# Kernel tuning notes

Measured on AMD Instinct MI355X. Metric: run time of the kernel, lower is better.

The kernel has to match this reference:

```python
import jax, jax.numpy as jnp
import numpy as np

B, T, L = 64, 128, 32          # batch, read timesteps, item_len (write phase)
D, R = 256, 1024               # output_dim (= input dim per step), controller rnn_size
N, M = 512, 128                # memory_rows, memory_columns
RH, WH = 1, 1                  # read / write heads
EPS = 1e-8
SCALE = 0.02


def setup_inputs() -> dict:
    key = jax.random.key(0)
    ks = jax.random.split(key, 6)
    in_dim = D + RH * M                      # controller sees [x_t, prev reads]
    head_dim = RH * (M + 6) + WH * (3 * M + 6)  # k,beta,g,s(3),gamma (+erase,add for write)
    return {
        "inputs": jax.random.normal(ks[0], (B, T, D), jnp.float32),
        "W_lstm": jax.random.normal(ks[1], (in_dim, 4 * R), jnp.float32) * SCALE,
        "U_lstm": jax.random.normal(ks[2], (R, 4 * R), jnp.float32) * SCALE,
        "b_lstm": jnp.zeros((4 * R,), jnp.float32),
        "W_heads": jax.random.normal(ks[3], (R, head_dim), jnp.float32) * SCALE,
        "b_heads": jnp.zeros((head_dim,), jnp.float32),
        "W_out": jax.random.normal(ks[4], (R + RH * M, D), jnp.float32) * SCALE,
        "b_out": jnp.zeros((D,), jnp.float32),
    }


def _address(Mem, Mem_norm, k, beta, g, s, gamma, w_prev):
    """NTM content + location addressing. Mem:[B,N,M], returns w:[B,N]."""
    k = jnp.tanh(k)                                   # [B,M]
    beta = jax.nn.softplus(beta)                      # [B,1]
    g = jax.nn.sigmoid(g)                             # [B,1]
    s = jax.nn.softmax(s, axis=-1)                    # [B,3] shifts (-1,0,1)
    gamma = 1.0 + jax.nn.softplus(gamma)              # [B,1]
    # cosine similarity content addressing
    sim = jnp.einsum('bnm,bm->bn', Mem, k) / (
        Mem_norm * jnp.linalg.norm(k, axis=-1, keepdims=True) + EPS)
    w_c = jax.nn.softmax(beta * sim, axis=-1)
    # interpolate with previous weighting
    w_g = g * w_c + (1.0 - g) * w_prev
    # circular convolutional shift over {-1,0,1}
    w_s = (s[:, 0:1] * jnp.roll(w_g, -1, axis=-1)
           + s[:, 1:2] * w_g
           + s[:, 2:3] * jnp.roll(w_g, 1, axis=-1))
    # sharpen
    w_pow = (w_s + EPS) ** gamma
    return w_pow / jnp.sum(w_pow, axis=-1, keepdims=True)


def _run(inputs, W_lstm, U_lstm, b_lstm, W_heads, b_heads, W_out, b_out):
    def step(carry, x_t):
        h, c, reads, w_r, w_w, Mem = carry
        # LSTM controller
        z = jnp.concatenate([x_t, reads], -1) @ W_lstm + h @ U_lstm + b_lstm
        zi, zf, zg, zo = jnp.split(z, 4, axis=-1)
        c = jax.nn.sigmoid(zf) * c + jax.nn.sigmoid(zi) * jnp.tanh(zg)
        h = jax.nn.sigmoid(zo) * jnp.tanh(c)
        # head parameters
        p = h @ W_heads + b_heads
        Mem_norm = jnp.linalg.norm(Mem, axis=-1)  # [B,N]
        new_w_r, new_reads = [], []
        for hh in range(RH):
            o = hh * (M + 6)
            w = _address(Mem, Mem_norm, p[:, o:o + M], p[:, o + M:o + M + 1],
                         p[:, o + M + 1:o + M + 2], p[:, o + M + 2:o + M + 5],
                         p[:, o + M + 5:o + M + 6], w_r[:, hh])
            new_w_r.append(w)
            new_reads.append(jnp.einsum('bn,bnm->bm', w, Mem))
        base, wsz = RH * (M + 6), 3 * M + 6
        new_w_w = []
        for hh in range(WH):
            o = base + hh * wsz
            w = _address(Mem, Mem_norm, p[:, o:o + M], p[:, o + M:o + M + 1],
                         p[:, o + M + 1:o + M + 2], p[:, o + M + 2:o + M + 5],
                         p[:, o + M + 5:o + M + 6], w_w[:, hh])
            erase = jax.nn.sigmoid(p[:, o + M + 6:o + 2 * M + 6])
            add = jnp.tanh(p[:, o + 2 * M + 6:o + 3 * M + 6])
            Mem = Mem * (1.0 - w[:, :, None] * erase[:, None, :]) + w[:, :, None] * add[:, None, :]
            new_w_w.append(w)
        reads = jnp.concatenate(new_reads, -1)
        out = jnp.concatenate([h, reads], -1) @ W_out + b_out
        carry = (h, c, reads, jnp.stack(new_w_r, 1), jnp.stack(new_w_w, 1), Mem)
        return carry, out

    init = (jnp.zeros((B, R)), jnp.zeros((B, R)), jnp.zeros((B, RH * M)),
            jnp.full((B, RH, N), 1.0 / N), jnp.full((B, WH, N), 1.0 / N),
            jnp.full((B, N, M), 1e-6))
    # read phase (inputs) followed by write phase (zero response sheet)
    xs = jnp.concatenate([inputs, jnp.zeros((B, L, D), inputs.dtype)], axis=1)
    xs = jnp.moveaxis(xs, 0, 1)  # [T+L, B, D]
    _, outs = jax.lax.scan(step, init, xs)
    write_outputs = jax.nn.sigmoid(jnp.moveaxis(outs[T:], 0, 1))  # [B, L, D]
    return write_outputs


def reference(inputs, W_lstm, U_lstm, b_lstm, W_heads, b_heads, W_out, b_out):
    return _run(inputs, W_lstm, U_lstm, b_lstm, W_heads, b_heads, W_out, b_out)
```

## Files before the change

### kernel.cpp

```cpp
#include <hip/hip_runtime.h>
#include <hip/hip_fp16.h>
#include <math.h>

#define B 64
#define T_READ 128
#define L_WRITE 32
#define TT 160
#define D 256
#define R 1024
#define N 512
#define M 128
#define HD 524
#define K5K 1152
#define EPS 1e-8f
#define BNM ((size_t)B*N*M)

__device__ __forceinline__ float sigmoidf(float x){ return 1.0f/(1.0f+expf(-x)); }
__device__ __forceinline__ float softplusf(float x){ return (x > 20.f) ? x : log1pf(expf(x)); }

__global__ __launch_bounds__(256) void kx_transpose(const float* __restrict__ x, float* __restrict__ xT){
    __shared__ float tile[64][65];
    const int t = blockIdx.x >> 2, k0 = (blockIdx.x & 3)*64;
    #pragma unroll
    for (int rep = 0; rep < 16; ++rep){
        int idx = rep*256 + threadIdx.x;
        int bl = idx >> 6, kl = idx & 63;
        tile[bl][kl] = x[((size_t)bl*T_READ + t)*D + k0 + kl];
    }
    __syncthreads();
    #pragma unroll
    for (int rep = 0; rep < 16; ++rep){
        int idx = rep*256 + threadIdx.x;
        int kl = idx >> 6, bl = idx & 63;
        xT[((size_t)t*D + k0 + kl)*64 + bl] = tile[bl][kl];
    }
}

__global__ __launch_bounds__(256) void kpack_w(const float* __restrict__ Wl, const float* __restrict__ Ul,
                                               __half* __restrict__ Wreh){
    const int k = blockIdx.x;
    const float* src = (k < 384) ? (Wl + (size_t)k*4096) : (Ul + (size_t)(k-384)*4096);
    #pragma unroll
    for (int it = 0; it < 16; ++it){
        int j = it*256 + threadIdx.x;
        int bk = j >> 4, r = j & 15, q = r >> 2, i = r & 3;
        Wreh[((size_t)bk*1408 + k)*16 + r] = __float2half_rn(src[q*1024 + bk*4 + i]);
    }
}

__global__ __launch_bounds__(256) void kpack_wh(const float* __restrict__ Wh, __half* __restrict__ Whh){
    const int k = blockIdx.x;
    for (int j = threadIdx.x; j < HD; j += 256)
        Whh[(size_t)k*HD + j] = __float2half_rn(Wh[(size_t)k*HD + j]);
}

__global__ void k_init(float* ht, float* c_t, float* reads_fin, float* wst, __half* Mem){
    size_t idx = (size_t)blockIdx.x*blockDim.x + threadIdx.x;
    size_t stride = (size_t)gridDim.x*blockDim.x;
    const __half mi = __float2half(1e-6f);
    for (size_t i = idx; i < BNM; i += stride) Mem[i] = mi;
    for (size_t i = idx; i < R*64; i += stride){ ht[i]=0.f; c_t[i]=0.f; }
    for (size_t i = idx; i < 2*128*64; i += stride) reads_fin[i] = 0.f;
    for (size_t i = idx; i < 4*B*N; i += stride) wst[i] = 1.f/512.f;
}

__global__ __launch_bounds__(1024) void k1_z(
    const float* __restrict__ xT, const __half* __restrict__ Wreh, const float* __restrict__ bl,
    float* __restrict__ ht, float* __restrict__ c_t, const float* __restrict__ reads_fin,
    float* __restrict__ hist, int t)
{
    __shared__ float comb[16384];
    const int bk = blockIdx.x;
    const int tid = threadIdx.x, lane = tid & 63, w = tid >> 6;
    const float* rf = reads_fin + (size_t)(t & 1)*8192;

    if (t > T_READ && bk < 8){
        int e = bk*1024 + tid;
        hist[((size_t)(t-1-T_READ)*K5K + 1024 + (e>>6))*64 + (e&63)] = rf[e];
    }

    const int r0 = bk*4;
    const int rd = (t < T_READ);
    const int kn = rd ? 88 : 72;
    const int k0 = rd ? w*88 : 256 + w*72;
    const __half* wbase = Wreh + ((size_t)bk*1408 + k0)*16;
    float acc[16];
    #pragma unroll
    for (int i = 0; i < 16; ++i) acc[i] = 0.f;
    #pragma unroll 4
    for (int kk = 0; kk < kn; ++kk){
        int k = k0 + kk;
        float a;
        if (k < 256)      a = xT[((size_t)t*256 + k)*64 + lane];
        else if (k < 384) a = rf[(k-256)*64 + lane];
        else              a = ht[(size_t)(k-384)*64 + lane];
        float4 raw0 = *reinterpret_cast<const float4*>(wbase + (size_t)kk*16);
        float4 raw1 = *reinterpret_cast<const float4*>(wbase + (size_t)kk*16 + 8);
        const __half2* h0 = reinterpret_cast<const __half2*>(&raw0);
        const __half2* h1 = reinterpret_cast<const __half2*>(&raw1);
        float2 f;
        f = __half22float2(h0[0]); acc[0] += a*f.x; acc[1] += a*f.y;
        f = __half22float2(h0[1]); acc[2] += a*f.x; acc[3] += a*f.y;
        f = __half22float2(h0[2]); acc[4] += a*f.x; acc[5] += a*f.y;
        f = __half22float2(h0[3]); acc[6] += a*f.x; acc[7] += a*f.y;
        f = __half22float2(h1[0]); acc[8] += a*f.x; acc[9] += a*f.y;
        f = __half22float2(h1[1]); acc[10]+= a*f.x; acc[11]+= a*f.y;
        f = __half22float2(h1[2]); acc[12]+= a*f.x; acc[13]+= a*f.y;
        f = __half22float2(h1[3]); acc[14]+= a*f.x; acc[15]+= a*f.y;
    }
    #pragma unroll
    for (int j = 0; j < 16; ++j) comb[(w*16 + j)*64 + lane] = acc[j];
    __syncthreads();
    if (tid < 256){
        int i = tid >> 6, b2 = tid & 63;
        float g4[4];
        #pragma unroll
        for (int q = 0; q < 4; ++q){
            float s = bl[q*1024 + r0 + i];
            #pragma unroll
            for (int ks = 0; ks < 16; ++ks) s += comb[(ks*16 + q*4 + i)*64 + b2];
            g4[q] = s;
        }
        int ri = (r0 + i)*64 + b2;
        float cn = sigmoidf(g4[1])*c_t[ri] + sigmoidf(g4[0])*tanhf(g4[2]);
        float hn = sigmoidf(g4[3])*tanhf(cn);
        c_t[ri] = cn;
        ht[ri] = hn;
        if (t >= T_READ) hist[((size_t)(t-T_READ)*K5K + r0 + i)*64 + b2] = hn;
    }
}

__global__ __launch_bounds__(1024) void k2f(
    const float* __restrict__ ht, const __half* __restrict__ Whh, const float* __restrict__ bh,
    float* __restrict__ khat, float* __restrict__ scal, float* __restrict__ eal)
{
    __shared__ float part[16][2][64];
    const int tid = threadIdx.x, lane = tid & 63, w = tid >> 6;
    const int col0 = blockIdx.x*2;
    const int k0 = w*64;
    float a0 = 0.f, a1 = 0.f;
    #pragma unroll 4
    for (int k = k0; k < k0+64; ++k){
        float a = ht[(size_t)k*64 + lane];
        __half2 wv = *reinterpret_cast<const __half2*>(Whh + (size_t)k*HD + col0);
        float2 f = __half22float2(wv);
        a0 += a*f.x; a1 += a*f.y;
    }
    part[w][0][lane] = a0;
    part[w][1][lane] = a1;
    __syncthreads();
    if (tid < 128){
        int c = tid >> 6, b = tid & 63;
        int col = col0 + c;
        float v = bh[col];
        #pragma unroll
        for (int w2 = 0; w2 < 16; ++w2) v += part[w2][c][b];
        if (col < 128)       khat[b*256 + col] = tanhf(v);
        else if (col < 134){ int i = col-128; scal[b*16 + i]     = (i==0)?softplusf(v):(i==1)?sigmoidf(v):(i==5)?1.f+softplusf(v):v; }
        else if (col < 262)  khat[b*256 + 128 + (col-134)] = tanhf(v);
        else if (col < 268){ int i = col-262; scal[b*16 + 8 + i] = (i==0)?softplusf(v):(i==1)?sigmoidf(v):(i==5)?1.f+softplusf(v):v; }
        else if (col < 396)  eal[b*256 + (col-268)]        = sigmoidf(v);
        else                 eal[b*256 + 128 + (col-396)]  = tanhf(v);
    }
}

__global__ __launch_bounds__(512) void k3_dots(
    const float* __restrict__ khat, const __half* __restrict__ Mem,
    float* __restrict__ mnorm, float* __restrict__ dots, float* __restrict__ reads_fin, int t)
{
    __shared__ float kh[256];
    const int b = blockIdx.x >> 3, nq = blockIdx.x & 7;
    const int tid = threadIdx.x, lane = tid & 63, w = tid >> 6;
    if (blockIdx.x < 8){
        int e = blockIdx.x*1024 + tid;
        reads_fin[(size_t)(t & 1)*8192 + e] = 0.f;
        reads_fin[(size_t)(t & 1)*8192 + e + 512] = 0.f;
    }
    if (tid < 256) kh[tid] = khat[b*256 + tid];
    __syncthreads();
    float2 kr  = reinterpret_cast<const float2*>(kh)[lane];
    float2 kw2 = reinterpret_cast<const float2*>(kh + 128)[lane];
    #pragma unroll 2
    for (int i = 0; i < 8; ++i){
        int n = nq*64 + w*8 + i;
        const __half* mrow = Mem + ((size_t)b*N + n)*M;
        __half2 mh = *reinterpret_cast<const __half2*>(mrow + lane*2);
        float2 mv = __half22float2(mh);
        float s2 = mv.x*mv.x + mv.y*mv.y;
        float dr = mv.x*kr.x + mv.y*kr.y;
        float dw = mv.x*kw2.x + mv.y*kw2.y;
        #pragma unroll
        for (int off = 32; off; off >>= 1){
            s2 += __shfl_xor(s2, off);
            dr += __shfl_xor(dr, off);
            dw += __shfl_xor(dw, off);
        }
        if (lane == 0){
            mnorm[b*N + n] = sqrtf(s2);
            dots[(b*2+0)*N + n] = dr;
            dots[(b*2+1)*N + n] = dw;
        }
    }
}

__device__ __forceinline__ float blk_sum8g(float v, volatile float* red8, int lane, int wgi){
    #pragma unroll
    for (int off = 32; off; off >>= 1) v += __shfl_xor(v, off);
    if (lane == 0) red8[wgi] = v;
    __syncthreads();
    float r = red8[0]+red8[1]+red8[2]+red8[3]+red8[4]+red8[5]+red8[6]+red8[7];
    __syncthreads();
    return r;
}
__device__ __forceinline__ float blk_max8g(float v, volatile float* red8, int lane, int wgi){
    #pragma unroll
    for (int off = 32; off; off >>= 1) v = fmaxf(v, __shfl_xor(v, off));
    if (lane == 0) red8[wgi] = v;
    __syncthreads();
    float r = fmaxf(fmaxf(fmaxf(red8[0],red8[1]),fmaxf(red8[2],red8[3])),
                    fmaxf(fmaxf(red8[4],red8[5]),fmaxf(red8[6],red8[7])));
    __syncthreads();
    return r;
}

__global__ __launch_bounds__(1024) void k4_addr(
    const float* __restrict__ khat, const float* __restrict__ scal, const float* __restrict__ ealg,
    const float* __restrict__ mnorm, const float* __restrict__ dots,
    float* __restrict__ wst, __half* __restrict__ Mem, float* __restrict__ reads_fin, int t)
{
    __shared__ float kh[256];
    __shared__ float sc[16];
    __shared__ float eal[256];
    __shared__ float wfin[1024];
    __shared__ float wgbuf[1024];
    __shared__ float red8[2][8];
    __shared__ float racc_s[1024];
    const int b = blockIdx.x >> 3, nq = blockIdx.x & 7;
    const int tid = threadIdx.x, lane = tid & 63;

    if (tid < 256)      kh[tid]      = khat[b*256 + tid];
    else if (tid < 272) sc[tid-256]  = scal[b*16 + (tid-256)];
    else if (tid < 528) eal[tid-272] = ealg[b*256 + (tid-272)];
    __syncthreads();

    {
        const int g = tid >> 9;
        const int n = tid & 511;
        const int wgi = (tid >> 6) & 7;
        float* wgl = wgbuf + g*512;
        volatile float* r8 = red8[g];

        float kv = (n < 128) ? kh[g*128 + n] : 0.f;
        float knm = sqrtf(blk_sum8g(kv*kv, r8, lane, wgi));
        float beta = sc[g*8+0], gg = sc[g*8+1], gamma = sc[g*8+5];
        float s0r = sc[g*8+2], s1r = sc[g*8+3], s2r = sc[g*8+4];
        float smx = fmaxf(s0r, fmaxf(s1r, s2r));
        float e0 = expf(s0r-smx), e1 = expf(s1r-smx), e2 = expf(s2r-smx);
        float esum = e0+e1+e2;
        float s0 = e0/esum, s1 = e1/esum, s2 = e2/esum;

        float sim = dots[(b*2+g)*N + n] / (mnorm[b*N + n]*knm + EPS);
        float aa = beta * sim;
        float amax = blk_max8g(aa, r8, lane, wgi);
        float ev = expf(aa - amax);
        float wc = ev / blk_sum8g(ev, r8, lane, wgi);

        const float* wpr = wst + ((size_t)((t&1)*2 + g))*(B*N);
        float*       wnx = wst + ((size_t)(((t+1)&1)*2 + g))*(B*N);
        float wprev = wpr[b*N + n];
        float wgv = gg*wc + (1.f - gg)*wprev;
        wgl[n] = wgv; __syncthreads();
        float wsv = s0*wgl[(n+1)&511] + s1*wgv + s2*wgl[(n-1)&511];
        float wp2 = powf(wsv + EPS, gamma);
        float wsum = blk_sum8g(wp2, r8, lane, wgi);
        float wv = wp2 / wsum;
        wfin[g*512 + n] = wv;
        if (nq == 0) wnx[b*N + n] = wv;
        __syncthreads();
    }

    {
        const int m = tid & 127, ns = tid >> 7;
        const float e  = eal[m];
        const float ad = eal[128 + m];
        float racc = 0.f;
        #pragma unroll 4
        for (int i2 = 0; i2 < 8; ++i2){
            int nn = nq*64 + i2*8 + ns;
            size_t idx = ((size_t)b*N + nn)*M + m;
            float v = __half2float(Mem[idx]);
            float wr = wfin[nn], ww = wfin[512 + nn];
            racc += wr*v;
            Mem[idx] = __float2half_rn(v*(1.f - ww*e) + ww*ad);
        }
        racc_s[tid] = racc;
        __syncthreads();
        if (tid < 128){
            float s = 0.f;
            #pragma unroll
            for (int g2 = 0; g2 < 8; ++g2) s += racc_s[g2*128 + tid];
            atomicAdd(&reads_fin[(size_t)((t+1) & 1)*8192 + tid*64 + b], s);
        }
    }
}

__global__ __launch_bounds__(256) void k_fin(const float* __restrict__ reads_fin, float* __restrict__ hist){
    int e = blockIdx.x*256 + threadIdx.x;
    float s = reads_fin[(size_t)(TT & 1)*8192 + e];
    hist[((size_t)31*K5K + 1024 + (e>>6))*64 + (e&63)] = s;
}

__global__ __launch_bounds__(512) void k5_out(
    const float* __restrict__ hist, const float* __restrict__ Wo, const float* __restrict__ bo,
    float* __restrict__ out)
{
    __shared__ float smem[16384];
    const int tid = threadIdx.x, lane = tid & 63, w = tid >> 6;
    const int l = blockIdx.x >> 3, jg = blockIdx.x & 7;
    const int j0 = jg*32;
    float acc[32];
    #pragma unroll
    for (int i = 0; i < 32; ++i) acc[i] = 0.f;
    const int k0 = w*144;
    #pragma unroll 2
    for (int kk = 0; kk < 144; ++kk){
        int k = k0 + kk;
        float a = hist[((size_t)l*K5K + k)*64 + lane];
        const float* wrow = Wo + (size_t)k*D + j0;
        #pragma unroll
        for (int qq = 0; qq < 8; ++qq){
            float4 wv = *reinterpret_cast<const float4*>(wrow + qq*4);
            acc[qq*4+0] += a*wv.x; acc[qq*4+1] += a*wv.y;
            acc[qq*4+2] += a*wv.z; acc[qq*4+3] += a*wv.w;
        }
    }
    __syncthreads();
    #pragma unroll
    for (int c = 0; c < 32; ++c) smem[(w*32 + c)*64 + lane] = acc[c];
    __syncthreads();
    {
        const int b2 = tid >> 3, jq = tid & 7;
        float4 ov;
        float* po = (float*)&ov;
        #pragma unroll
        for (int i = 0; i < 4; ++i){
            int c = jq*4 + i;
            float s = bo[j0 + c];
            #pragma unroll
            for (int ks = 0; ks < 8; ++ks) s += smem[(ks*32 + c)*64 + b2];
            po[i] = sigmoidf(s);
        }
        *reinterpret_cast<float4*>(out + ((size_t)b2*L_WRITE + l)*D + j0 + jq*4) = ov;
    }
}

extern "C" void kernel_launch(void* const* d_in, const int* in_sizes, int n_in,
                              void* d_out, int out_size, void* d_ws, size_t ws_size,
                              hipStream_t stream)
{
    const float* x   = (const float*)d_in[0];
    const float* Wl  = (const float*)d_in[1];
    const float* Ul  = (const float*)d_in[2];
    const float* bl  = (const float*)d_in[3];
    const float* Wh  = (const float*)d_in[4];
    const float* bh  = (const float*)d_in[5];
    const float* Wo  = (const float*)d_in[6];
    const float* bo  = (const float*)d_in[7];
    float* out = (float*)d_out;

    float* ws = (float*)d_ws;
    float* xT    = ws; ws += (size_t)T_READ*D*64;
    __half* Wreh = (__half*)ws; ws += (size_t)1408*4096/2;
    __half* Whh  = (__half*)ws; ws += (size_t)1024*HD/2 + 64;
    float* ht    = ws; ws += (size_t)R*64;
    float* c_t   = ws; ws += (size_t)R*64;
    float* khat  = ws; ws += (size_t)B*256;
    float* scal  = ws; ws += (size_t)B*16;
    float* eal   = ws; ws += (size_t)B*256;
    float* mnorm = ws; ws += (size_t)B*N;
    float* dots  = ws; ws += (size_t)B*2*N;
    float* wst   = ws; ws += (size_t)4*B*N;
    __half* Mem  = (__half*)ws; ws += BNM/2;
    float* reads_fin = ws; ws += (size_t)2*128*64;
    float* hist  = ws; ws += (size_t)L_WRITE*K5K*64;

    hipLaunchKernelGGL(kx_transpose, dim3(T_READ*4), dim3(256), 0, stream, x, xT);
    hipLaunchKernelGGL(kpack_w,      dim3(1408),     dim3(256), 0, stream, Wl, Ul, Wreh);
    hipLaunchKernelGGL(kpack_wh,     dim3(1024),     dim3(256), 0, stream, Wh, Whh);
    hipLaunchKernelGGL(k_init,       dim3(2048),     dim3(256), 0, stream, ht, c_t, reads_fin, wst, Mem);

    for (int t = 0; t < TT; ++t){
        hipLaunchKernelGGL(k1_z,    dim3(256), dim3(1024), 0, stream, xT, Wreh, bl, ht, c_t, reads_fin, hist, t);
        hipLaunchKernelGGL(k2f,     dim3(262), dim3(1024), 0, stream, ht, Whh, bh, khat, scal, eal);
        hipLaunchKernelGGL(k3_dots, dim3(512), dim3(512),  0, stream, khat, Mem, mnorm, dots, reads_fin, t);
        hipLaunchKernelGGL(k4_addr, dim3(512), dim3(1024), 0, stream, khat, scal, eal, mnorm, dots, wst, Mem, reads_fin, t);
    }
    hipLaunchKernelGGL(k_fin,  dim3(32),  dim3(256), 0, stream, reads_fin, hist);
    hipLaunchKernelGGL(k5_out, dim3(256), dim3(512), 0, stream, hist, Wo, bo, out);
}
```

Baseline: 10.63 ms.

## Fuse memory-row dot products into the addressing kernel and drop k3

Removes the separate k3_dots launch. Each addressing block now computes the row norms and the key dot products for all 512 memory rows of its batch directly into shared memory. This saves one kernel launch per timestep and the global write/read round trip for mnorm and dots. The cost is that each of the 8 blocks per batch re-reads the full memory matrix for its batch, so memory traffic per step rises about 8x; those reads may be served from cache. Zeroing of reads_fin moves into k2f.

```diff
diff --git a/kernel.cpp b/kernel.cpp
--- a/kernel.cpp
+++ b/kernel.cpp
@@ -132,11 +132,16 @@
 
 __global__ __launch_bounds__(1024) void k2f(
     const float* __restrict__ ht, const __half* __restrict__ Whh, const float* __restrict__ bh,
-    float* __restrict__ khat, float* __restrict__ scal, float* __restrict__ eal)
+    float* __restrict__ khat, float* __restrict__ scal, float* __restrict__ eal,
+    float* __restrict__ reads_fin, int t)
 {
     __shared__ float part[16][2][64];
     const int tid = threadIdx.x, lane = tid & 63, w = tid >> 6;
     const int col0 = blockIdx.x*2;
+    if (blockIdx.x < 8){
+        int e = blockIdx.x*1024 + tid;
+        reads_fin[(size_t)(t & 1)*8192 + e] = 0.f;
+    }
     const int k0 = w*64;
     float a0 = 0.f, a1 = 0.f;
     #pragma unroll 4
@@ -164,45 +169,6 @@
     }
 }
 
-__global__ __launch_bounds__(512) void k3_dots(
-    const float* __restrict__ khat, const __half* __restrict__ Mem,
-    float* __restrict__ mnorm, float* __restrict__ dots, float* __restrict__ reads_fin, int t)
-{
-    __shared__ float kh[256];
-    const int b = blockIdx.x >> 3, nq = blockIdx.x & 7;
-    const int tid = threadIdx.x, lane = tid & 63, w = tid >> 6;
-    if (blockIdx.x < 8){
-        int e = blockIdx.x*1024 + tid;
-        reads_fin[(size_t)(t & 1)*8192 + e] = 0.f;
-        reads_fin[(size_t)(t & 1)*8192 + e + 512] = 0.f;
-    }
-    if (tid < 256) kh[tid] = khat[b*256 + tid];
-    __syncthreads();
-    float2 kr  = reinterpret_cast<const float2*>(kh)[lane];
-    float2 kw2 = reinterpret_cast<const float2*>(kh + 128)[lane];
-    #pragma unroll 2
-    for (int i = 0; i < 8; ++i){
-        int n = nq*64 + w*8 + i;
-        const __half* mrow = Mem + ((size_t)b*N + n)*M;
-        __half2 mh = *reinterpret_cast<const __half2*>(mrow + lane*2);
-        float2 mv = __half22float2(mh);
-        float s2 = mv.x*mv.x + mv.y*mv.y;
-        float dr = mv.x*kr.x + mv.y*kr.y;
-        float dw = mv.x*kw2.x + mv.y*kw2.y;
-        #pragma unroll
-        for (int off = 32; off; off >>= 1){
-            s2 += __shfl_xor(s2, off);
-            dr += __shfl_xor(dr, off);
-            dw += __shfl_xor(dw, off);
-        }
-        if (lane == 0){
-            mnorm[b*N + n] = sqrtf(s2);
-            dots[(b*2+0)*N + n] = dr;
-            dots[(b*2+1)*N + n] = dw;
-        }
-    }
-}
-
 __device__ __forceinline__ float blk_sum8g(float v, volatile float* red8, int lane, int wgi){
     #pragma unroll
     for (int off = 32; off; off >>= 1) v += __shfl_xor(v, off);
@@ -223,14 +189,15 @@
     return r;
 }
 
-__global__ __launch_bounds__(1024) void k4_addr(
+__global__ __launch_bounds__(1024) void k34_mem(
     const float* __restrict__ khat, const float* __restrict__ scal, const float* __restrict__ ealg,
-    const float* __restrict__ mnorm, const float* __restrict__ dots,
     float* __restrict__ wst, __half* __restrict__ Mem, float* __restrict__ reads_fin, int t)
 {
     __shared__ float kh[256];
     __shared__ float sc[16];
     __shared__ float eal[256];
+    __shared__ float mnorm_s[512];
+    __shared__ float dots_s[2][512];
     __shared__ float wfin[1024];
     __shared__ float wgbuf[1024];
     __shared__ float red8[2][8];
@@ -241,6 +208,33 @@
     if (tid < 256)      kh[tid]      = khat[b*256 + tid];
     else if (tid < 272) sc[tid-256]  = scal[b*16 + (tid-256)];
     else if (tid < 528) eal[tid-272] = ealg[b*256 + (tid-272)];
+    __syncthreads();
+
+    {
+        const int w16 = tid >> 6;
+        float2 kr  = reinterpret_cast<const float2*>(kh)[lane];
+        float2 kw2 = reinterpret_cast<const float2*>(kh + 128)[lane];
+        #pragma unroll 2
+        for (int i = 0; i < 32; ++i){
+            int n = w16*32 + i;
+            __half2 mh = *reinterpret_cast<const __half2*>(Mem + ((size_t)b*N + n)*M + lane*2);
+            float2 mv = __half22float2(mh);
+            float s2 = mv.x*mv.x + mv.y*mv.y;
+            float dr = mv.x*kr.x + mv.y*kr.y;
+            float dw = mv.x*kw2.x + mv.y*kw2.y;
+            #pragma unroll
+            for (int off = 32; off; off >>= 1){
+                s2 += __shfl_xor(s2, off);
+                dr += __shfl_xor(dr, off);
+                dw += __shfl_xor(dw, off);
+            }
+            if (lane == 0){
+                mnorm_s[n] = sqrtf(s2);
+                dots_s[0][n] = dr;
+                dots_s[1][n] = dw;
+            }
+        }
+    }
     __syncthreads();
 
     {
@@ -259,7 +253,7 @@
         float esum = e0+e1+e2;
         float s0 = e0/esum, s1 = e1/esum, s2 = e2/esum;
 
-        float sim = dots[(b*2+g)*N + n] / (mnorm[b*N + n]*knm + EPS);
+        float sim = dots_s[g][n] / (mnorm_s[n]*knm + EPS);
         float aa = beta * sim;
         float amax = blk_max8g(aa, r8, lane, wgi);
         float ev = expf(aa - amax);
@@ -377,8 +371,6 @@
     float* khat  = ws; ws += (size_t)B*256;
     float* scal  = ws; ws += (size_t)B*16;
     float* eal   = ws; ws += (size_t)B*256;
-    float* mnorm = ws; ws += (size_t)B*N;
-    float* dots  = ws; ws += (size_t)B*2*N;
     float* wst   = ws; ws += (size_t)4*B*N;
     __half* Mem  = (__half*)ws; ws += BNM/2;
     float* reads_fin = ws; ws += (size_t)2*128*64;
@@ -391,9 +383,8 @@
 
     for (int t = 0; t < TT; ++t){
         hipLaunchKernelGGL(k1_z,    dim3(256), dim3(1024), 0, stream, xT, Wreh, bl, ht, c_t, reads_fin, hist, t);
-        hipLaunchKernelGGL(k2f,     dim3(262), dim3(1024), 0, stream, ht, Whh, bh, khat, scal, eal);
-        hipLaunchKernelGGL(k3_dots, dim3(512), dim3(512),  0, stream, khat, Mem, mnorm, dots, reads_fin, t);
-        hipLaunchKernelGGL(k4_addr, dim3(512), dim3(1024), 0, stream, khat, scal, eal, mnorm, dots, wst, Mem, reads_fin, t);
+        hipLaunchKernelGGL(k2f,     dim3(262), dim3(1024), 0, stream, ht, Whh, bh, khat, scal, eal, reads_fin, t);
+        hipLaunchKernelGGL(k34_mem, dim3(512), dim3(1024), 0, stream, khat, scal, eal, wst, Mem, reads_fin, t);
     }
     hipLaunchKernelGGL(k_fin,  dim3(32),  dim3(256), 0, stream, reads_fin, hist);
     hipLaunchKernelGGL(k5_out, dim3(256), dim3(512), 0, stream, hist, Wo, bo, out);
```

New measurement: 18.27 ms. 1.72x slower.
